# Kernel tuning notes

Hardware: AMD Instinct MI355X
Metric: run time of the kernel (lower is better)

The kernel has to match this reference:

```python
import jax, jax.numpy as jnp
import numpy as np

NEG_INF = -9e15  # matches torch's -9000000000000000.0 mask fill
LEAKY_SLOPE = 0.01  # F.leaky_relu default


def setup_inputs() -> dict:
    key = jax.random.key(0)
    ks = jax.random.split(key, 6)
    B, N, F_in, F_out = 4, 4096, 256, 128
    h = jax.random.normal(ks[0], (B, N, F_in), dtype=jnp.float32)
    adj = jax.random.randint(ks[1], (B, N, N), 0, 2, dtype=jnp.int32)
    W_w = jax.random.normal(ks[2], (F_out, F_in), dtype=jnp.float32) * (1.0 / np.sqrt(F_in))
    W_b = jax.random.normal(ks[3], (F_out,), dtype=jnp.float32) * 0.01
    a_w = jax.random.normal(ks[4], (2 * F_out,), dtype=jnp.float32) * (1.0 / np.sqrt(2 * F_out))
    a_b = jax.random.normal(ks[5], (), dtype=jnp.float32) * 0.01
    return {"h": h, "adj": adj, "W_w": W_w, "W_b": W_b, "a_w": a_w, "a_b": a_b}


def reference(h, adj, W_w, W_b, a_w, a_b):
    # Wh: [B, N, F_out]
    Wh = jnp.einsum('bnf,of->bno', h, W_w) + W_b
    F_out = Wh.shape[-1]
    # a([Wh_i, Wh_j]) decomposes as a_src.Wh_i + a_dst.Wh_j + a_b (linearity),
    # avoiding the O(N^2 * 2F) repeat+cat intermediate while computing identical math.
    a_src, a_dst = a_w[:F_out], a_w[F_out:]
    src = jnp.einsum('bno,o->bn', Wh, a_src)  # [B, N]
    dst = jnp.einsum('bno,o->bn', Wh, a_dst)  # [B, N]
    e = src[:, :, None] + dst[:, None, :] + a_b  # [B, N, N]
    e = jnp.where(e >= 0, e, LEAKY_SLOPE * e)  # leaky_relu
    masked = jnp.where(adj > 0, e, NEG_INF)
    attention = jax.nn.softmax(masked, axis=-1)  # row softmax over neighbors j
    h_prime = jnp.einsum('bij,bjo->bio', attention, Wh)
    return h_prime
```

## Files before the change

kernel.cpp:

```cpp
#include <hip/hip_runtime.h>
#include <hip/hip_bf16.h>

typedef __attribute__((ext_vector_type(4))) float f32x4;
typedef __attribute__((ext_vector_type(8))) short s16x8;
typedef unsigned long long u64;

#define NB_ 4
#define N_ 4096
#define FI_ 256
#define FO_ 128
#define NROWS 16384
#define SPLIT 4
#define NSTEPS ((N_ / SPLIT) / 32)

__device__ __forceinline__ unsigned pkbf(float a, float b) {
    __hip_bfloat162 t = __float22bfloat162_rn(make_float2(a, b));
    unsigned r; __builtin_memcpy(&r, &t, 4); return r;
}

typedef __attribute__((address_space(1))) const void CGV;
typedef __attribute__((address_space(3))) void LDSV;
__device__ __forceinline__ void gload16(const void* g, void* l) {
    __builtin_amdgcn_global_load_lds((CGV*)g, (LDSV*)l, 16, 0, 0);
}

__global__ __launch_bounds__(256) void k0_packw(
    const float* __restrict__ Ww, __hip_bfloat16* __restrict__ whi,
    __hip_bfloat16* __restrict__ wlo)
{
    int idx = blockIdx.x * 256 + threadIdx.x;
    float v = Ww[idx];
    __hip_bfloat16 hi = __float2bfloat16(v);
    whi[idx] = hi;
    wlo[idx] = __float2bfloat16(v - __bfloat162float(hi));
}

__global__ __launch_bounds__(256) void k1_wh(
    const float* __restrict__ h, const __hip_bfloat16* __restrict__ whi,
    const __hip_bfloat16* __restrict__ wlo, const float* __restrict__ Wb,
    const float* __restrict__ aw, const float* __restrict__ ab,
    short* __restrict__ WhTf, float* __restrict__ srcv,
    float* __restrict__ dstbv, unsigned* __restrict__ auxp)
{
    __shared__ float lds[16][132];
    const int tid = threadIdx.x;
    const int w = tid >> 6, l = tid & 63;
    const int lr = l & 15, g = l >> 4;
    const int r0 = blockIdx.x * 16;
    const float* hp = h + (size_t)(r0 + lr) * FI_ + g * 8;

    f32x4 acc[2] = {(f32x4)0.f, (f32x4)0.f};

    #pragma unroll
    for (int kt = 0; kt < 8; ++kt) {
        f32x4 x0 = *(const f32x4*)(hp + kt * 32);
        f32x4 x1 = *(const f32x4*)(hp + kt * 32 + 4);
        float xx[8];
        #pragma unroll
        for (int t = 0; t < 4; ++t) { xx[t] = x0[t]; xx[t + 4] = x1[t]; }
        union { s16x8 v; unsigned u[4]; } ahi, alo;
        #pragma unroll
        for (int t = 0; t < 4; ++t) {
            float a0 = xx[2 * t], a1 = xx[2 * t + 1];
            unsigned uh = pkbf(a0, a1);
            ahi.u[t] = uh;
            float h0f = __uint_as_float(uh << 16);
            float h1f = __uint_as_float(uh & 0xffff0000u);
            alo.u[t] = pkbf(a0 - h0f, a1 - h1f);
        }
        #pragma unroll
        for (int c = 0; c < 2; ++c) {
            const int o = w * 32 + c * 16 + lr;
            s16x8 bh = *(const s16x8*)(whi + (size_t)o * FI_ + kt * 32 + g * 8);
            s16x8 bl = *(const s16x8*)(wlo + (size_t)o * FI_ + kt * 32 + g * 8);
            acc[c] = __builtin_amdgcn_mfma_f32_16x16x32_bf16(ahi.v, bh, acc[c], 0, 0, 0);
            acc[c] = __builtin_amdgcn_mfma_f32_16x16x32_bf16(alo.v, bh, acc[c], 0, 0, 0);
            acc[c] = __builtin_amdgcn_mfma_f32_16x16x32_bf16(ahi.v, bl, acc[c], 0, 0, 0);
        }
    }

    #pragma unroll
    for (int c = 0; c < 2; ++c) {
        int col = w * 32 + c * 16 + lr;
        float wb = Wb[col];
        #pragma unroll
        for (int kk = 0; kk < 4; ++kk)
            lds[g * 4 + kk][col] = acc[c][kk] + wb;
    }
    __syncthreads();

    {
        const int o = tid >> 1, joct = tid & 1;
        const int jblk = (r0 & 4095) >> 5;
        const int bb = r0 >> 12;
        const int lb = ((r0 >> 3) & 3) + joct;
        union { s16x8 v; unsigned u[4]; } af;
        #pragma unroll
        for (int q = 0; q < 4; ++q)
            af.u[q] = pkbf(lds[joct * 8 + 2 * q][o], lds[joct * 8 + 2 * q + 1][o]);
        short* dst = WhTf + (((size_t)bb * 128 + jblk) * 8 + (o >> 4)) * 512
                          + ((o & 15) + 16 * lb) * 8;
        *(s16x8*)dst = af.v;
    }

    {
        const int row = tid >> 4, seg = tid & 15;
        float sp = 0.f, dp = 0.f;
        #pragma unroll
        for (int i = 0; i < 8; ++i) {
            float v = lds[row][seg * 8 + i];
            sp += v * aw[seg * 8 + i];
            dp += v * aw[FO_ + seg * 8 + i];
        }
        #pragma unroll
        for (int off = 8; off >= 1; off >>= 1) {
            sp += __shfl_xor(sp, off);
            dp += __shfl_xor(dp, off);
        }
        if (seg == 0) {
            int r = r0 + row;
            srcv[r] = sp;
            float db = dp + ab[0];
            dstbv[r] = db;
            auxp[r] = pkbf(__expf(db), __expf(0.01f * db));
        }
    }
}

__global__ __launch_bounds__(256) void k2b_max(
    const float* __restrict__ dstbv, float* __restrict__ maxv)
{
    const int b = blockIdx.x;
    const int t = threadIdx.x, w = t >> 6, l = t & 63;
    float m = -3.4e38f;
    for (int i = t; i < N_; i += 256) m = fmaxf(m, dstbv[b * N_ + i]);
    #pragma unroll
    for (int off = 32; off >= 1; off >>= 1) m = fmaxf(m, __shfl_xor(m, off));
    __shared__ float red[4];
    if (l == 0) red[w] = m;
    __syncthreads();
    if (t == 0) maxv[b] = fmaxf(fmaxf(red[0], red[1]), fmaxf(red[2], red[3]));
}

__global__ __launch_bounds__(256, 4) void k3_gat(
    const int* __restrict__ adj, const short* __restrict__ WhTf,
    const float* __restrict__ srcv, const unsigned* __restrict__ auxp,
    const float* __restrict__ maxv, float* __restrict__ pacc,
    float* __restrict__ prow)
{
    __shared__ int adjb[2][64][32];
    __shared__ __hip_bfloat16 whb[2][4096];
    __shared__ float rsum[64];

    const int t = threadIdx.x;
    const int w = t >> 6, l = t & 63;
    const int lr = l & 15, g = l >> 4;
    const int rh = w & 1, oh = w >> 1;
    const int b = blockIdx.x >> 6;
    const int rblk = (blockIdx.x & 63) * 64;
    const int bN = b * N_;
    const int j0 = blockIdx.y * (N_ / SPLIT);

    float C1[2], C2[2];
    {
        const float mdb = maxv[b];
        #pragma unroll
        for (int rt = 0; rt < 2; ++rt) {
            int r = rblk + rh * 32 + rt * 16 + lr;
            float s = srcv[bN + r];
            float eub = s + mdb;
            float m = fmaxf(eub, 0.01f * eub);
            C1[rt] = __expf(s - m);
            C2[rt] = __expf(0.01f * s - m);
        }
    }

    const unsigned* axp = auxp + (size_t)bN + j0 + g * 8;
    const short* whsrc = WhTf + ((size_t)b * 128 + (j0 >> 5)) * 4096;

    f32x4 acc[2][4];
    #pragma unroll
    for (int rt = 0; rt < 2; ++rt)
        #pragma unroll
        for (int ot = 0; ot < 4; ++ot) acc[rt][ot] = (f32x4)0.f;
    float rs0 = 0.f, rs1 = 0.f;

    auto stage_adj = [&](int bi, int s) {
        const int jb = j0 + s * 32;
        #pragma unroll
        for (int i = 0; i < 2; ++i) {
            int r = (t >> 3) + i * 32;
            int c = t & 7;
            const int* src = adj + (size_t)(bN + rblk + r) * N_ + jb
                                 + ((c ^ (r & 7)) << 2);
            gload16(src, &adjb[bi][0][0] + (size_t)(i * 256 + w * 64) * 4);
        }
    };
    auto stage_wh = [&](int bi, int s) {
        const short* src = whsrc + (size_t)s * 4096;
        #pragma unroll
        for (int i = 0; i < 2; ++i)
            gload16(src + (size_t)(i * 256 + t) * 8,
                    &whb[bi][0] + (size_t)(i * 256 + w * 64) * 8);
    };

    uint4 xc0, xc1;
    stage_adj(0, 0);
    stage_wh(0, 0);
    xc0 = *(const uint4*)(axp);
    xc1 = *(const uint4*)(axp + 4);
    __syncthreads();
    int cur = 0;

    for (int s = 0; s < NSTEPS; ++s) {
        uint4 xn0 = {0, 0, 0, 0}, xn1 = {0, 0, 0, 0};
        const bool more = (s + 1 < NSTEPS);
        if (more) {
            stage_adj(cur ^ 1, s + 1);
            stage_wh(cur ^ 1, s + 1);
            const int jn = (s + 1) * 32;
            xn0 = *(const uint4*)(axp + jn);
            xn1 = *(const uint4*)(axp + jn + 4);
        }

        const unsigned ax[8] = {xc0.x, xc0.y, xc0.z, xc0.w,
                                xc1.x, xc1.y, xc1.z, xc1.w};
        float e1f[8], e2f[8];
        #pragma unroll
        for (int e = 0; e < 8; ++e) {
            e1f[e] = __uint_as_float(ax[e] << 16);
            e2f[e] = __uint_as_float(ax[e] & 0xffff0000u);
        }
        s16x8 Bf[4];
        #pragma unroll
        for (int ot = 0; ot < 4; ++ot)
            Bf[ot] = *(const s16x8*)&whb[cur][(size_t)((oh * 4 + ot) * 64 + l) * 8];

        #pragma unroll
        for (int rt = 0; rt < 2; ++rt) {
            const int R = rh * 32 + rt * 16 + lr;
            const int4 a0 = *(const int4*)&adjb[cur][R][((2 * g) ^ (lr & 7)) << 2];
            const int4 a1 = *(const int4*)&adjb[cur][R][((2 * g + 1) ^ (lr & 7)) << 2];
            const int av[8] = {a0.x, a0.y, a0.z, a0.w, a1.x, a1.y, a1.z, a1.w};
            float p[8];
            #pragma unroll
            for (int e = 0; e < 8; ++e) {
                float v = fmaxf(e1f[e] * C1[rt], e2f[e] * C2[rt]);
                p[e] = (av[e] > 0) ? v : 0.f;
                if (rt == 0) rs0 += p[e]; else rs1 += p[e];
            }
            union { s16x8 v; unsigned u[4]; } af;
            af.u[0] = pkbf(p[0], p[1]); af.u[1] = pkbf(p[2], p[3]);
            af.u[2] = pkbf(p[4], p[5]); af.u[3] = pkbf(p[6], p[7]);
            #pragma unroll
            for (int ot = 0; ot < 4; ++ot)
                acc[rt][ot] = __builtin_amdgcn_mfma_f32_16x16x32_bf16(
                    af.v, Bf[ot], acc[rt][ot], 0, 0, 0);
        }

        __syncthreads();
        xc0 = xn0; xc1 = xn1;
        cur ^= 1;
    }

    rs0 += __shfl_xor(rs0, 16); rs0 += __shfl_xor(rs0, 32);
    rs1 += __shfl_xor(rs1, 16); rs1 += __shfl_xor(rs1, 32);
    if (oh == 0 && l < 16) {
        rsum[rh * 32 + l] = rs0;
        rsum[rh * 32 + 16 + l] = rs1;
    }
    __syncthreads();

    const size_t sb = (size_t)blockIdx.y * ((size_t)NROWS * FO_);
    #pragma unroll
    for (int rt = 0; rt < 2; ++rt) {
        #pragma unroll
        for (int kk = 0; kk < 4; ++kk) {
            int rloc = rh * 32 + rt * 16 + g * 4 + kk;
            int grow = bN + rblk + rloc;
            float* pp = pacc + sb + (size_t)grow * FO_ + oh * 64 + lr;
            #pragma unroll
            for (int ot = 0; ot < 4; ++ot)
                pp[ot * 16] = acc[rt][ot][kk];
            if (oh == 0 && lr == 0)
                prow[blockIdx.y * NROWS + grow] = rsum[rloc];
        }
    }
}

__global__ __launch_bounds__(256) void k4_comb(
    const float* __restrict__ pacc, const float* __restrict__ prow,
    float* __restrict__ out)
{
    const int idx = blockIdx.x * 256 + threadIdx.x;
    const int grow = idx >> 7;
    float s = 0.f, rs = 0.f;
    #pragma unroll
    for (int si = 0; si < SPLIT; ++si) {
        s  += pacc[(size_t)si * ((size_t)NROWS * FO_) + idx];
        rs += prow[si * NROWS + grow];
    }
    out[idx] = s / rs;
}

extern "C" void kernel_launch(void* const* d_in, const int* in_sizes, int n_in,
                              void* d_out, int out_size, void* d_ws, size_t ws_size,
                              hipStream_t stream)
{
    const float* h  = (const float*)d_in[0];
    const int* adj  = (const int*)d_in[1];
    const float* Ww = (const float*)d_in[2];
    const float* Wb = (const float*)d_in[3];
    const float* aw = (const float*)d_in[4];
    const float* ab = (const float*)d_in[5];
    float* out = (float*)d_out;

    char* wsb = (char*)d_ws;
    float* pacc          = (float*)wsb;
    short* WhTf          = (short*)(wsb + 33554432u);
    char* aux            = wsb + 37748736u;
    float* srcv          = (float*)(aux);
    float* dstbv         = (float*)(aux + (64u << 10));
    unsigned* auxp       = (unsigned*)(aux + (128u << 10));
    __hip_bfloat16* whi  = (__hip_bfloat16*)(aux + (192u << 10));
    __hip_bfloat16* wlo  = (__hip_bfloat16*)(aux + (256u << 10));
    float* maxv          = (float*)(aux + (320u << 10));
    float* prow          = (float*)(aux + (384u << 10));

    k0_packw<<<128, 256, 0, stream>>>(Ww, whi, wlo);
    k1_wh<<<1024, 256, 0, stream>>>(h, whi, wlo, Wb, aw, ab, WhTf, srcv, dstbv, auxp);
    k2b_max<<<4, 256, 0, stream>>>(dstbv, maxv);
    dim3 g3(NB_ * 64, SPLIT);
    k3_gat<<<g3, 256, 0, stream>>>(adj, WhTf, srcv, auxp, maxv, pacc, prow);
    k4_comb<<<8192, 256, 0, stream>>>(pacc, prow, out);
}
```

Before: 130.8 us.

## Load Wh B-fragments directly to registers and triple-buffer adjacency prefetch

The Wh B-operand no longer goes through LDS; each wave loads its fragments straight from global memory into registers one step ahead. The adjacency tile moves to a three-slot LDS ring, prefetched two steps ahead and guarded by a manual vmcnt wait plus s_barrier, which replaces the trailing __syncthreads. This aims to hide global latency better, cut the per-step LDS traffic and remove one barrier per step. In exchange it raises register pressure, and the hard-coded vmcnt(6) count depends on the exact number of outstanding loads, which makes it fragile.

```diff
diff --git a/kernel.cpp b/kernel.cpp
--- a/kernel.cpp
+++ b/kernel.cpp
@@ -148,8 +148,7 @@
     const float* __restrict__ maxv, float* __restrict__ pacc,
     float* __restrict__ prow)
 {
-    __shared__ int adjb[2][64][32];
-    __shared__ __hip_bfloat16 whb[2][4096];
+    __shared__ int adjb[3][64][32];
     __shared__ float rsum[64];
 
     const int t = threadIdx.x;
@@ -196,32 +195,45 @@
             gload16(src, &adjb[bi][0][0] + (size_t)(i * 256 + w * 64) * 4);
         }
     };
-    auto stage_wh = [&](int bi, int s) {
-        const short* src = whsrc + (size_t)s * 4096;
-        #pragma unroll
-        for (int i = 0; i < 2; ++i)
-            gload16(src + (size_t)(i * 256 + t) * 8,
-                    &whb[bi][0] + (size_t)(i * 256 + w * 64) * 8);
+    auto loadB = [&](int s, s16x8* Bv) {
+        const short* p = whsrc + (size_t)s * 4096;
+        #pragma unroll
+        for (int ot = 0; ot < 4; ++ot)
+            Bv[ot] = *(const s16x8*)(p + (oh * 4 + ot) * 512 + l * 8);
     };
 
     uint4 xc0, xc1;
+    s16x8 Bc[4];
     stage_adj(0, 0);
-    stage_wh(0, 0);
+    __builtin_amdgcn_sched_barrier(0);
     xc0 = *(const uint4*)(axp);
     xc1 = *(const uint4*)(axp + 4);
-    __syncthreads();
-    int cur = 0;
+    loadB(0, Bc);
+    __builtin_amdgcn_sched_barrier(0);
+    stage_adj(1, 1);
+    __builtin_amdgcn_sched_barrier(0);
+
+    int rA = 0, rB = 1, rC = 2;
 
     for (int s = 0; s < NSTEPS; ++s) {
+        __builtin_amdgcn_sched_barrier(0);
+        asm volatile("s_waitcnt vmcnt(6)" ::: "memory");
+        __builtin_amdgcn_sched_barrier(0);
+        __builtin_amdgcn_s_barrier();
+        __builtin_amdgcn_sched_barrier(0);
+
         uint4 xn0 = {0, 0, 0, 0}, xn1 = {0, 0, 0, 0};
+        s16x8 Bn[4];
         const bool more = (s + 1 < NSTEPS);
         if (more) {
-            stage_adj(cur ^ 1, s + 1);
-            stage_wh(cur ^ 1, s + 1);
             const int jn = (s + 1) * 32;
             xn0 = *(const uint4*)(axp + jn);
             xn1 = *(const uint4*)(axp + jn + 4);
-        }
+            loadB(s + 1, Bn);
+        }
+        __builtin_amdgcn_sched_barrier(0);
+        if (s + 2 < NSTEPS) stage_adj(rC, s + 2);
+        __builtin_amdgcn_sched_barrier(0);
 
         const unsigned ax[8] = {xc0.x, xc0.y, xc0.z, xc0.w,
                                 xc1.x, xc1.y, xc1.z, xc1.w};
@@ -231,16 +243,11 @@
             e1f[e] = __uint_as_float(ax[e] << 16);
             e2f[e] = __uint_as_float(ax[e] & 0xffff0000u);
         }
-        s16x8 Bf[4];
-        #pragma unroll
-        for (int ot = 0; ot < 4; ++ot)
-            Bf[ot] = *(const s16x8*)&whb[cur][(size_t)((oh * 4 + ot) * 64 + l) * 8];
-
         #pragma unroll
         for (int rt = 0; rt < 2; ++rt) {
             const int R = rh * 32 + rt * 16 + lr;
-            const int4 a0 = *(const int4*)&adjb[cur][R][((2 * g) ^ (lr & 7)) << 2];
-            const int4 a1 = *(const int4*)&adjb[cur][R][((2 * g + 1) ^ (lr & 7)) << 2];
+            const int4 a0 = *(const int4*)&adjb[rA][R][((2 * g) ^ (lr & 7)) << 2];
+            const int4 a1 = *(const int4*)&adjb[rA][R][((2 * g + 1) ^ (lr & 7)) << 2];
             const int av[8] = {a0.x, a0.y, a0.z, a0.w, a1.x, a1.y, a1.z, a1.w};
             float p[8];
             #pragma unroll
@@ -255,12 +262,15 @@
             #pragma unroll
             for (int ot = 0; ot < 4; ++ot)
                 acc[rt][ot] = __builtin_amdgcn_mfma_f32_16x16x32_bf16(
-                    af.v, Bf[ot], acc[rt][ot], 0, 0, 0);
-        }
-
-        __syncthreads();
-        xc0 = xn0; xc1 = xn1;
-        cur ^= 1;
+                    af.v, Bc[ot], acc[rt][ot], 0, 0, 0);
+        }
+
+        if (more) {
+            xc0 = xn0; xc1 = xn1;
+            #pragma unroll
+            for (int ot = 0; ot < 4; ++ot) Bc[ot] = Bn[ot];
+        }
+        int tmp = rA; rA = rB; rB = rC; rC = tmp;
     }
 
     rs0 += __shfl_xor(rs0, 16); rs0 += __shfl_xor(rs0, 32);
```

New measurement: 136.2 us. +4.1%, slower.

## Halve GAT row tile, widen adj chunk, read Wh fragments directly from global

Applied to the files above, without the earlier changes.

The attention kernel now handles 32 rows per block instead of 64, doubling the grid, and stages 128-column adjacency chunks into LDS rather than 32-column ones. The Wh B-fragments and per-column aux values are read straight from global memory (relying on cache) instead of being double-buffered through LDS. This cuts LDS footprint and barrier count per column and may raise occupancy. In exchange each Wh tile is loaded by twice as many blocks, and the global fragment loads sit directly in front of the MFMAs with no prefetch.

```diff
diff --git a/kernel.cpp b/kernel.cpp
--- a/kernel.cpp
+++ b/kernel.cpp
@@ -11,7 +11,8 @@
 #define FO_ 128
 #define NROWS 16384
 #define SPLIT 4
-#define NSTEPS ((N_ / SPLIT) / 32)
+#define PHC 128
+#define NST ((N_ / SPLIT) / PHC)
 
 __device__ __forceinline__ unsigned pkbf(float a, float b) {
     __hip_bfloat162 t = __float22bfloat162_rn(make_float2(a, b));
@@ -148,143 +149,114 @@
     const float* __restrict__ maxv, float* __restrict__ pacc,
     float* __restrict__ prow)
 {
-    __shared__ int adjb[2][64][32];
-    __shared__ __hip_bfloat16 whb[2][4096];
-    __shared__ float rsum[64];
+    __shared__ int adjb[2][32][128];
+    __shared__ float rsum[32];
 
     const int t = threadIdx.x;
     const int w = t >> 6, l = t & 63;
     const int lr = l & 15, g = l >> 4;
     const int rh = w & 1, oh = w >> 1;
-    const int b = blockIdx.x >> 6;
-    const int rblk = (blockIdx.x & 63) * 64;
+    const int b = blockIdx.x >> 7;
+    const int rblk = (blockIdx.x & 127) * 32;
     const int bN = b * N_;
     const int j0 = blockIdx.y * (N_ / SPLIT);
 
-    float C1[2], C2[2];
+    float C1, C2;
     {
-        const float mdb = maxv[b];
-        #pragma unroll
-        for (int rt = 0; rt < 2; ++rt) {
-            int r = rblk + rh * 32 + rt * 16 + lr;
-            float s = srcv[bN + r];
-            float eub = s + mdb;
-            float m = fmaxf(eub, 0.01f * eub);
-            C1[rt] = __expf(s - m);
-            C2[rt] = __expf(0.01f * s - m);
-        }
+        int r = rblk + rh * 16 + lr;
+        float s = srcv[bN + r];
+        float eub = s + maxv[b];
+        float m = fmaxf(eub, 0.01f * eub);
+        C1 = __expf(s - m);
+        C2 = __expf(0.01f * s - m);
     }
 
     const unsigned* axp = auxp + (size_t)bN + j0 + g * 8;
     const short* whsrc = WhTf + ((size_t)b * 128 + (j0 >> 5)) * 4096;
 
-    f32x4 acc[2][4];
-    #pragma unroll
-    for (int rt = 0; rt < 2; ++rt)
-        #pragma unroll
-        for (int ot = 0; ot < 4; ++ot) acc[rt][ot] = (f32x4)0.f;
-    float rs0 = 0.f, rs1 = 0.f;
+    f32x4 acc[4];
+    #pragma unroll
+    for (int ot = 0; ot < 4; ++ot) acc[ot] = (f32x4)0.f;
+    float rs = 0.f;
 
     auto stage_adj = [&](int bi, int s) {
-        const int jb = j0 + s * 32;
-        #pragma unroll
-        for (int i = 0; i < 2; ++i) {
-            int r = (t >> 3) + i * 32;
-            int c = t & 7;
+        const int jb = j0 + s * PHC;
+        #pragma unroll
+        for (int i = 0; i < 4; ++i) {
+            int slot = i * 64 + (t & 63) + (t >> 6) * 256;
+            int r = (i * 256 + t) >> 5;
+            int c = (i * 256 + t) & 31;
             const int* src = adj + (size_t)(bN + rblk + r) * N_ + jb
                                  + ((c ^ (r & 7)) << 2);
+            (void)slot;
             gload16(src, &adjb[bi][0][0] + (size_t)(i * 256 + w * 64) * 4);
         }
     };
-    auto stage_wh = [&](int bi, int s) {
-        const short* src = whsrc + (size_t)s * 4096;
-        #pragma unroll
-        for (int i = 0; i < 2; ++i)
-            gload16(src + (size_t)(i * 256 + t) * 8,
-                    &whb[bi][0] + (size_t)(i * 256 + w * 64) * 8);
-    };
-
-    uint4 xc0, xc1;
+
     stage_adj(0, 0);
-    stage_wh(0, 0);
-    xc0 = *(const uint4*)(axp);
-    xc1 = *(const uint4*)(axp + 4);
     __syncthreads();
     int cur = 0;
 
-    for (int s = 0; s < NSTEPS; ++s) {
-        uint4 xn0 = {0, 0, 0, 0}, xn1 = {0, 0, 0, 0};
-        const bool more = (s + 1 < NSTEPS);
-        if (more) {
-            stage_adj(cur ^ 1, s + 1);
-            stage_wh(cur ^ 1, s + 1);
-            const int jn = (s + 1) * 32;
-            xn0 = *(const uint4*)(axp + jn);
-            xn1 = *(const uint4*)(axp + jn + 4);
-        }
-
-        const unsigned ax[8] = {xc0.x, xc0.y, xc0.z, xc0.w,
-                                xc1.x, xc1.y, xc1.z, xc1.w};
-        float e1f[8], e2f[8];
-        #pragma unroll
-        for (int e = 0; e < 8; ++e) {
-            e1f[e] = __uint_as_float(ax[e] << 16);
-            e2f[e] = __uint_as_float(ax[e] & 0xffff0000u);
-        }
-        s16x8 Bf[4];
-        #pragma unroll
-        for (int ot = 0; ot < 4; ++ot)
-            Bf[ot] = *(const s16x8*)&whb[cur][(size_t)((oh * 4 + ot) * 64 + l) * 8];
-
-        #pragma unroll
-        for (int rt = 0; rt < 2; ++rt) {
-            const int R = rh * 32 + rt * 16 + lr;
-            const int4 a0 = *(const int4*)&adjb[cur][R][((2 * g) ^ (lr & 7)) << 2];
-            const int4 a1 = *(const int4*)&adjb[cur][R][((2 * g + 1) ^ (lr & 7)) << 2];
+    for (int s = 0; s < NST; ++s) {
+        if (s + 1 < NST) stage_adj(cur ^ 1, s + 1);
+
+        #pragma unroll
+        for (int js = 0; js < 4; ++js) {
+            const int jc = s * PHC + js * 32;
+            uint4 x0 = *(const uint4*)(axp + jc);
+            uint4 x1 = *(const uint4*)(axp + jc + 4);
+            const short* bp = whsrc + (size_t)(s * 4 + js) * 4096;
+            s16x8 Bf[4];
+            #pragma unroll
+            for (int ot = 0; ot < 4; ++ot)
+                Bf[ot] = *(const s16x8*)(bp + (oh * 4 + ot) * 512 + l * 8);
+
+            const int R = rh * 16 + lr;
+            const int c0 = js * 8 + 2 * g;
+            const int4 a0 = *(const int4*)&adjb[cur][R][(c0 ^ (R & 7)) << 2];
+            const int4 a1 = *(const int4*)&adjb[cur][R][((c0 + 1) ^ (R & 7)) << 2];
+
+            const unsigned ax[8] = {x0.x, x0.y, x0.z, x0.w, x1.x, x1.y, x1.z, x1.w};
             const int av[8] = {a0.x, a0.y, a0.z, a0.w, a1.x, a1.y, a1.z, a1.w};
             float p[8];
             #pragma unroll
             for (int e = 0; e < 8; ++e) {
-                float v = fmaxf(e1f[e] * C1[rt], e2f[e] * C2[rt]);
+                float e1f = __uint_as_float(ax[e] << 16);
+                float e2f = __uint_as_float(ax[e] & 0xffff0000u);
+                float v = fmaxf(e1f * C1, e2f * C2);
                 p[e] = (av[e] > 0) ? v : 0.f;
-                if (rt == 0) rs0 += p[e]; else rs1 += p[e];
+                rs += p[e];
             }
             union { s16x8 v; unsigned u[4]; } af;
             af.u[0] = pkbf(p[0], p[1]); af.u[1] = pkbf(p[2], p[3]);
             af.u[2] = pkbf(p[4], p[5]); af.u[3] = pkbf(p[6], p[7]);
+
             #pragma unroll
             for (int ot = 0; ot < 4; ++ot)
-                acc[rt][ot] = __builtin_amdgcn_mfma_f32_16x16x32_bf16(
-                    af.v, Bf[ot], acc[rt][ot], 0, 0, 0);
+                acc[ot] = __builtin_amdgcn_mfma_f32_16x16x32_bf16(
+                    af.v, Bf[ot], acc[ot], 0, 0, 0);
         }
 
         __syncthreads();
-        xc0 = xn0; xc1 = xn1;
         cur ^= 1;
     }
 
-    rs0 += __shfl_xor(rs0, 16); rs0 += __shfl_xor(rs0, 32);
-    rs1 += __shfl_xor(rs1, 16); rs1 += __shfl_xor(rs1, 32);
-    if (oh == 0 && l < 16) {
-        rsum[rh * 32 + l] = rs0;
-        rsum[rh * 32 + 16 + l] = rs1;
-    }
+    rs += __shfl_xor(rs, 16);
+    rs += __shfl_xor(rs, 32);
+    if (oh == 0 && l < 16) rsum[rh * 16 + l] = rs;
     __syncthreads();
 
     const size_t sb = (size_t)blockIdx.y * ((size_t)NROWS * FO_);
     #pragma unroll
-    for (int rt = 0; rt < 2; ++rt) {
-        #pragma unroll
-        for (int kk = 0; kk < 4; ++kk) {
-            int rloc = rh * 32 + rt * 16 + g * 4 + kk;
-            int grow = bN + rblk + rloc;
-            float* pp = pacc + sb + (size_t)grow * FO_ + oh * 64 + lr;
-            #pragma unroll
-            for (int ot = 0; ot < 4; ++ot)
-                pp[ot * 16] = acc[rt][ot][kk];
-            if (oh == 0 && lr == 0)
-                prow[blockIdx.y * NROWS + grow] = rsum[rloc];
-        }
+    for (int kk = 0; kk < 4; ++kk) {
+        int rloc = rh * 16 + g * 4 + kk;
+        int grow = bN + rblk + rloc;
+        float* pp = pacc + sb + (size_t)grow * FO_ + oh * 64 + lr;
+        #pragma unroll
+        for (int ot = 0; ot < 4; ++ot)
+            pp[ot * 16] = acc[ot][kk];
+        if (oh == 0 && lr == 0)
+            prow[blockIdx.y * NROWS + grow] = rsum[rloc];
     }
 }
 
@@ -330,7 +302,7 @@
     k0_packw<<<128, 256, 0, stream>>>(Ww, whi, wlo);
     k1_wh<<<1024, 256, 0, stream>>>(h, whi, wlo, Wb, aw, ab, WhTf, srcv, dstbv, auxp);
     k2b_max<<<4, 256, 0, stream>>>(dstbv, maxv);
-    dim3 g3(NB_ * 64, SPLIT);
+    dim3 g3(NB_ * 128, SPLIT);
     k3_gat<<<g3, 256, 0, stream>>>(adj, WhTf, srcv, auxp, maxv, pacc, prow);
     k4_comb<<<8192, 256, 0, stream>>>(pacc, prow, out);
 }
```

Measured after the change: 142.9 us. 1.09x slower.

## Pre-pack adjacency into bitmasks and drop LDS staging in attention kernel

Applied to the files above, without the earlier changes.

Adds a kernel that streams the int32 adjacency matrix once and packs it into 64-bit ballot bitmasks per row. The attention kernel then reads these compact bits and the Wh tiles straight from global memory into registers. This removes the double-buffered LDS staging and the per-step block barrier. The full adjacency read still happens, now in a separate launch, and Wh reads now depend on L2/global latency rather than LDS.

```diff
diff --git a/kernel.cpp b/kernel.cpp
--- a/kernel.cpp
+++ b/kernel.cpp
@@ -18,10 +18,25 @@
     unsigned r; __builtin_memcpy(&r, &t, 4); return r;
 }
 
-typedef __attribute__((address_space(1))) const void CGV;
-typedef __attribute__((address_space(3))) void LDSV;
-__device__ __forceinline__ void gload16(const void* g, void* l) {
-    __builtin_amdgcn_global_load_lds((CGV*)g, (LDSV*)l, 16, 0, 0);
+__global__ __launch_bounds__(256) void k_adjb(
+    const int* __restrict__ adj, u64* __restrict__ bits)
+{
+    const int w = threadIdx.x >> 6, l = threadIdx.x & 63;
+    const int row = blockIdx.x * 4 + w;
+    const int* ar = adj + (size_t)row * N_;
+    u64 mine = 0;
+    #pragma unroll
+    for (int s0 = 0; s0 < 64; s0 += 8) {
+        int v[8];
+        #pragma unroll
+        for (int q = 0; q < 8; ++q) v[q] = ar[(s0 + q) * 64 + l];
+        #pragma unroll
+        for (int q = 0; q < 8; ++q) {
+            u64 bm = __ballot(v[q] > 0);
+            if (l == s0 + q) mine = bm;
+        }
+    }
+    bits[(size_t)row * 64 + l] = mine;
 }
 
 __global__ __launch_bounds__(256) void k0_packw(
@@ -143,13 +158,11 @@
 }
 
 __global__ __launch_bounds__(256, 4) void k3_gat(
-    const int* __restrict__ adj, const short* __restrict__ WhTf,
+    const u64* __restrict__ bits, const short* __restrict__ WhTf,
     const float* __restrict__ srcv, const unsigned* __restrict__ auxp,
     const float* __restrict__ maxv, float* __restrict__ pacc,
     float* __restrict__ prow)
 {
-    __shared__ int adjb[2][64][32];
-    __shared__ __hip_bfloat16 whb[2][4096];
     __shared__ float rsum[64];
 
     const int t = threadIdx.x;
@@ -161,20 +174,23 @@
     const int bN = b * N_;
     const int j0 = blockIdx.y * (N_ / SPLIT);
 
-    float C1[2], C2[2];
+    float C1r[2], C2r[2];
+    int row[2];
     {
         const float mdb = maxv[b];
         #pragma unroll
         for (int rt = 0; rt < 2; ++rt) {
-            int r = rblk + rh * 32 + rt * 16 + lr;
-            float s = srcv[bN + r];
+            row[rt] = rblk + rh * 32 + rt * 16 + lr;
+            float s = srcv[bN + row[rt]];
             float eub = s + mdb;
             float m = fmaxf(eub, 0.01f * eub);
-            C1[rt] = __expf(s - m);
-            C2[rt] = __expf(0.01f * s - m);
-        }
-    }
-
+            C1r[rt] = __expf(s - m);
+            C2r[rt] = __expf(0.01f * s - m);
+        }
+    }
+
+    const u64* bitp0 = bits + (size_t)(bN + row[0]) * 64 + (j0 >> 6);
+    const u64* bitp1 = bits + (size_t)(bN + row[1]) * 64 + (j0 >> 6);
     const unsigned* axp = auxp + (size_t)bN + j0 + g * 8;
     const short* whsrc = WhTf + ((size_t)b * 128 + (j0 >> 5)) * 4096;
 
@@ -185,89 +201,66 @@
         for (int ot = 0; ot < 4; ++ot) acc[rt][ot] = (f32x4)0.f;
     float rs0 = 0.f, rs1 = 0.f;
 
-    auto stage_adj = [&](int bi, int s) {
-        const int jb = j0 + s * 32;
-        #pragma unroll
-        for (int i = 0; i < 2; ++i) {
-            int r = (t >> 3) + i * 32;
-            int c = t & 7;
-            const int* src = adj + (size_t)(bN + rblk + r) * N_ + jb
-                                 + ((c ^ (r & 7)) << 2);
-            gload16(src, &adjb[bi][0][0] + (size_t)(i * 256 + w * 64) * 4);
-        }
-    };
-    auto stage_wh = [&](int bi, int s) {
-        const short* src = whsrc + (size_t)s * 4096;
-        #pragma unroll
-        for (int i = 0; i < 2; ++i)
-            gload16(src + (size_t)(i * 256 + t) * 8,
-                    &whb[bi][0] + (size_t)(i * 256 + w * 64) * 8);
-    };
-
-    uint4 xc0, xc1;
-    stage_adj(0, 0);
-    stage_wh(0, 0);
-    xc0 = *(const uint4*)(axp);
-    xc1 = *(const uint4*)(axp + 4);
-    __syncthreads();
-    int cur = 0;
+    u64 bc0 = bitp0[0], bc1 = bitp1[0];
+    u64 bn0 = 0, bn1 = 0;
+    uint4 xc0 = *(const uint4*)(axp);
+    uint4 xc1 = *(const uint4*)(axp + 4);
 
     for (int s = 0; s < NSTEPS; ++s) {
+        const short* bp = whsrc + (size_t)s * 4096;
+        s16x8 Bf[4];
+        #pragma unroll
+        for (int ot = 0; ot < 4; ++ot)
+            Bf[ot] = *(const s16x8*)(bp + (oh * 4 + ot) * 512 + l * 8);
+
         uint4 xn0 = {0, 0, 0, 0}, xn1 = {0, 0, 0, 0};
-        const bool more = (s + 1 < NSTEPS);
-        if (more) {
-            stage_adj(cur ^ 1, s + 1);
-            stage_wh(cur ^ 1, s + 1);
-            const int jn = (s + 1) * 32;
-            xn0 = *(const uint4*)(axp + jn);
-            xn1 = *(const uint4*)(axp + jn + 4);
-        }
-
+        if (s + 1 < NSTEPS) {
+            xn0 = *(const uint4*)(axp + (s + 1) * 32);
+            xn1 = *(const uint4*)(axp + (s + 1) * 32 + 4);
+        }
+        if ((s & 1) == 0 && s + 2 < NSTEPS) {
+            bn0 = bitp0[(s >> 1) + 1];
+            bn1 = bitp1[(s >> 1) + 1];
+        }
+
+        const int sh = ((s & 1) << 5) + g * 8;
+        const unsigned m0 = (unsigned)(bc0 >> sh) & 0xFFu;
+        const unsigned m1 = (unsigned)(bc1 >> sh) & 0xFFu;
         const unsigned ax[8] = {xc0.x, xc0.y, xc0.z, xc0.w,
                                 xc1.x, xc1.y, xc1.z, xc1.w};
-        float e1f[8], e2f[8];
+        float p0[8], p1[8];
         #pragma unroll
         for (int e = 0; e < 8; ++e) {
-            e1f[e] = __uint_as_float(ax[e] << 16);
-            e2f[e] = __uint_as_float(ax[e] & 0xffff0000u);
-        }
-        s16x8 Bf[4];
-        #pragma unroll
-        for (int ot = 0; ot < 4; ++ot)
-            Bf[ot] = *(const s16x8*)&whb[cur][(size_t)((oh * 4 + ot) * 64 + l) * 8];
-
-        #pragma unroll
-        for (int rt = 0; rt < 2; ++rt) {
-            const int R = rh * 32 + rt * 16 + lr;
-            const int4 a0 = *(const int4*)&adjb[cur][R][((2 * g) ^ (lr & 7)) << 2];
-            const int4 a1 = *(const int4*)&adjb[cur][R][((2 * g + 1) ^ (lr & 7)) << 2];
-            const int av[8] = {a0.x, a0.y, a0.z, a0.w, a1.x, a1.y, a1.z, a1.w};
-            float p[8];
-            #pragma unroll
-            for (int e = 0; e < 8; ++e) {
-                float v = fmaxf(e1f[e] * C1[rt], e2f[e] * C2[rt]);
-                p[e] = (av[e] > 0) ? v : 0.f;
-                if (rt == 0) rs0 += p[e]; else rs1 += p[e];
-            }
-            union { s16x8 v; unsigned u[4]; } af;
-            af.u[0] = pkbf(p[0], p[1]); af.u[1] = pkbf(p[2], p[3]);
-            af.u[2] = pkbf(p[4], p[5]); af.u[3] = pkbf(p[6], p[7]);
-            #pragma unroll
-            for (int ot = 0; ot < 4; ++ot)
-                acc[rt][ot] = __builtin_amdgcn_mfma_f32_16x16x32_bf16(
-                    af.v, Bf[ot], acc[rt][ot], 0, 0, 0);
-        }
-
-        __syncthreads();
+            float e1f = __uint_as_float(ax[e] << 16);
+            float e2f = __uint_as_float(ax[e] & 0xffff0000u);
+            float v0 = fmaxf(e1f * C1r[0], e2f * C2r[0]);
+            float v1 = fmaxf(e1f * C1r[1], e2f * C2r[1]);
+            p0[e] = ((m0 >> e) & 1u) ? v0 : 0.f;
+            p1[e] = ((m1 >> e) & 1u) ? v1 : 0.f;
+            rs0 += p0[e];
+            rs1 += p1[e];
+        }
+        union { s16x8 v; unsigned u[4]; } af0, af1;
+        af0.u[0] = pkbf(p0[0], p0[1]); af0.u[1] = pkbf(p0[2], p0[3]);
+        af0.u[2] = pkbf(p0[4], p0[5]); af0.u[3] = pkbf(p0[6], p0[7]);
+        af1.u[0] = pkbf(p1[0], p1[1]); af1.u[1] = pkbf(p1[2], p1[3]);
+        af1.u[2] = pkbf(p1[4], p1[5]); af1.u[3] = pkbf(p1[6], p1[7]);
+
+        #pragma unroll
+        for (int ot = 0; ot < 4; ++ot) {
+            acc[0][ot] = __builtin_amdgcn_mfma_f32_16x16x32_bf16(af0.v, Bf[ot], acc[0][ot], 0, 0, 0);
+            acc[1][ot] = __builtin_amdgcn_mfma_f32_16x16x32_bf16(af1.v, Bf[ot], acc[1][ot], 0, 0, 0);
+        }
+
         xc0 = xn0; xc1 = xn1;
-        cur ^= 1;
+        if (s & 1) { bc0 = bn0; bc1 = bn1; }
     }
 
     rs0 += __shfl_xor(rs0, 16); rs0 += __shfl_xor(rs0, 32);
     rs1 += __shfl_xor(rs1, 16); rs1 += __shfl_xor(rs1, 32);
-    if (oh == 0 && l < 16) {
-        rsum[rh * 32 + l] = rs0;
-        rsum[rh * 32 + 16 + l] = rs1;
+    if (oh == 0 && g == 0) {
+        rsum[rh * 32 + lr] = rs0;
+        rsum[rh * 32 + 16 + lr] = rs1;
     }
     __syncthreads();
 
@@ -318,7 +311,8 @@
     char* wsb = (char*)d_ws;
     float* pacc          = (float*)wsb;
     short* WhTf          = (short*)(wsb + 33554432u);
-    char* aux            = wsb + 37748736u;
+    u64* bits            = (u64*)(wsb + 37748736u);
+    char* aux            = wsb + 46137344u;
     float* srcv          = (float*)(aux);
     float* dstbv         = (float*)(aux + (64u << 10));
     unsigned* auxp       = (unsigned*)(aux + (128u << 10));
@@ -327,10 +321,11 @@
     float* maxv          = (float*)(aux + (320u << 10));
     float* prow          = (float*)(aux + (384u << 10));
 
+    k_adjb<<<4096, 256, 0, stream>>>(adj, bits);
     k0_packw<<<128, 256, 0, stream>>>(Ww, whi, wlo);
     k1_wh<<<1024, 256, 0, stream>>>(h, whi, wlo, Wb, aw, ab, WhTf, srcv, dstbv, auxp);
     k2b_max<<<4, 256, 0, stream>>>(dstbv, maxv);
     dim3 g3(NB_ * 64, SPLIT);
-    k3_gat<<<g3, 256, 0, stream>>>(adj, WhTf, srcv, auxp, maxv, pacc, prow);
+    k3_gat<<<g3, 256, 0, stream>>>(bits, WhTf, srcv, auxp, maxv, pacc, prow);
     k4_comb<<<8192, 256, 0, stream>>>(pacc, prow, out);
 }
```

Measured after the change: 145.0 us. 1.11x slower.
